# Performance work log

Measured on AMD Instinct MI355X. Metric: run time of the kernel, lower is better.

Reference implementation:

```python
import jax, jax.numpy as jnp
import numpy as np

B, T, C, H = 4, 4096, 1024, 64

def setup_inputs() -> dict:
    key = jax.random.key(0)
    kx, kq, kk, kv = jax.random.split(key, 4)
    x  = jax.random.normal(kx, (B, T, C), dtype=jnp.float32)
    # nn.Linear(C, H, bias=False) weights have shape [H, C]; y = x @ W.T
    Wq = jax.random.normal(kq, (H, C), dtype=jnp.float32) * (C ** -0.5)
    Wk = jax.random.normal(kk, (H, C), dtype=jnp.float32) * (C ** -0.5)
    Wv = jax.random.normal(kv, (H, C), dtype=jnp.float32) * (C ** -0.5)
    return {"x": x, "Wq": Wq, "Wk": Wk, "Wv": Wv}

def reference(x, Wq, Wk, Wv):
    T_ = x.shape[1]
    scale = jnp.asarray(Wq.shape[0] ** -0.5, dtype=x.dtype)
    q = jnp.einsum('btc,hc->bth', x, Wq)
    k = jnp.einsum('btc,hc->bth', x, Wk)
    v = jnp.einsum('btc,hc->bth', x, Wv)
    w = jnp.einsum('bqh,bkh->bqk', q, k)  # [B, T, T] scores
    causal = jnp.tril(jnp.ones((T_, T_), dtype=bool))
    # original: masked_fill(-inf) then scale; -inf * scale == -inf, so equivalent
    w = jnp.where(causal, w * scale, -jnp.inf)
    w = jax.nn.softmax(w, axis=-1)
    # dropout p=0.0 (eval/deterministic): identity
    return jnp.einsum('bqk,bkh->bqh', w, v)
```

## Files before the change

kernel.cpp:

```cpp
#include <hip/hip_runtime.h>
#include <hip/hip_bf16.h>

#define B_ 4
#define T_ 4096
#define C_ 1024

typedef __bf16 bf16_t;
typedef __bf16 bf16x8 __attribute__((ext_vector_type(8)));
typedef float f32x4 __attribute__((ext_vector_type(4)));

__device__ __forceinline__ void gld16(const void* g, void* l) {
    __builtin_amdgcn_global_load_lds((const __attribute__((address_space(1))) void*)g,
                                     (__attribute__((address_space(3))) void*)l, 16, 0, 0);
}

__global__ void wcvt_kernel(const float* __restrict__ Wq, const float* __restrict__ Wk,
                            const float* __restrict__ Wv, bf16_t* __restrict__ wbf) {
    int i = blockIdx.x * 256 + threadIdx.x;
    int m = i >> 16;
    int r = i & 65535;
    const float* src = (m == 0) ? Wq : (m == 1) ? Wk : Wv;
    float s = (m == 0) ? 0.125f * 1.44269504f : 1.0f;
    wbf[i] = (bf16_t)(src[r] * s);
}

__global__ __launch_bounds__(256, 2)
void qkv_proj_kernel(const float* __restrict__ x, const bf16_t* __restrict__ wbf,
                     bf16_t* __restrict__ qb, bf16_t* __restrict__ kb,
                     bf16_t* __restrict__ vtb) {
    __shared__ bf16_t wsb[3][12288];

    const int tid = threadIdx.x;
    const int w = tid >> 6, lane = tid & 63, lr = lane & 15, kg = lane >> 4;
    const int rg = w & 1, cg = w >> 1;
    const int row0 = blockIdx.x * 32;

    const float* xr = x + (size_t)(row0 + rg * 16 + lr) * 1024 + kg * 8;

#define STAGE_W(kk, sl) {                                                           \
        _Pragma("unroll")                                                           \
        for (int j = 0; j < 6; ++j) {                                               \
            int idx = tid + j * 256; int h = idx >> 3, u = idx & 7;                 \
            gld16((const char*)wbf + (size_t)h * 2048 + (size_t)(kk) * 128          \
                      + ((u ^ (h & 7)) * 16),                                       \
                  (char*)&wsb[sl][0] + (size_t)idx * 16); } }
#define LOADX(kk, sl) {                                                             \
        xb[sl][0] = *(const float4*)(xr + (kk) * 64);                               \
        xb[sl][1] = *(const float4*)(xr + (kk) * 64 + 4);                           \
        xb[sl][2] = *(const float4*)(xr + (kk) * 64 + 32);                          \
        xb[sl][3] = *(const float4*)(xr + (kk) * 64 + 36); }

    float4 xb[3][4];
    f32x4 acc[6];
    #pragma unroll
    for (int j = 0; j < 6; ++j) acc[j] = (f32x4){0.f, 0.f, 0.f, 0.f};

    STAGE_W(0, 0); LOADX(0, 0);
    STAGE_W(1, 1); LOADX(1, 1);

    #pragma unroll
    for (int c = 0; c < 16; ++c) {
        if (c < 15) {
            asm volatile("s_waitcnt vmcnt(10)" ::: "memory");
        } else {
            asm volatile("s_waitcnt vmcnt(0)" ::: "memory");
        }
        __builtin_amdgcn_s_barrier();
        if (c + 2 < 16) {
            STAGE_W(c + 2, (c + 2) % 3);
            LOADX(c + 2, (c + 2) % 3);
        }

        {
            const int cur = c % 3;
            const bf16_t* wst = &wsb[cur][0];
            bf16x8 af[2];
            #pragma unroll
            for (int s = 0; s < 2; ++s) {
                float4 a0 = xb[cur][s * 2];
                float4 a1 = xb[cur][s * 2 + 1];
                af[s][0]=(bf16_t)a0.x; af[s][1]=(bf16_t)a0.y;
                af[s][2]=(bf16_t)a0.z; af[s][3]=(bf16_t)a0.w;
                af[s][4]=(bf16_t)a1.x; af[s][5]=(bf16_t)a1.y;
                af[s][6]=(bf16_t)a1.z; af[s][7]=(bf16_t)a1.w;
            }
            __builtin_amdgcn_s_setprio(1);
            #pragma unroll
            for (int j = 0; j < 6; ++j) {
                int p = cg * 6 + j;
                #pragma unroll
                for (int s = 0; s < 2; ++s) {
                    bf16x8 bfr = *(const bf16x8*)&wst[(p * 16 + lr) * 64
                                                      + (((4 * s + kg) ^ (lr & 7)) * 8)];
                    acc[j] = __builtin_amdgcn_mfma_f32_16x16x32_bf16(af[s], bfr, acc[j], 0, 0, 0);
                }
            }
            __builtin_amdgcn_s_setprio(0);
        }
    }

    #pragma unroll
    for (int j = 0; j < 6; ++j) {
        int p = cg * 6 + j;
        int m = p >> 2;
        int h = (p & 3) * 16 + lr;
        #pragma unroll
        for (int i = 0; i < 4; ++i) {
            int t = row0 + rg * 16 + kg * 4 + i;
            float v = acc[j][i];
            if (m == 0) {
                qb[(size_t)t * 64 + h] = (bf16_t)v;
            } else if (m == 1) {
                kb[(size_t)t * 64 + ((((h >> 3) ^ (t & 7)) << 3) | (h & 7))] = (bf16_t)v;
            } else {
                int bb = t >> 12, tt = t & 4095;
                vtb[(size_t)(bb * 64 + h) * 4096 + (tt & ~63)
                    + (((((tt >> 3) & 7) ^ (h & 7))) << 3) + (tt & 7)] = (bf16_t)v;
            }
        }
    }
#undef STAGE_W
#undef LOADX
}

__global__ __launch_bounds__(256, 2)
void attn_kernel(const bf16_t* __restrict__ qb, const bf16_t* __restrict__ kb,
                 const bf16_t* __restrict__ vtb, float* __restrict__ out) {
    __shared__ bf16_t kvb[2][2][8192];
    __shared__ bf16_t p_lds[4][16][68];

    const int tid = threadIdx.x;
    const int w = tid >> 6, lane = tid & 63, lr = lane & 15, kg = lane >> 4;
    const int rg = w & 1, slice = w >> 1;
    const int bid = blockIdx.x;
    const int b = bid & 3;
    const int qt = 127 - (bid >> 2);
    const int qrow0 = qt * 32 + rg * 16;
    const size_t bT = (size_t)b * 4096;

    const int nch    = (qt + 2) >> 1;
    const int nsteps = (nch + 1) >> 1;

#define STAGE_CHUNK(kk, pp, cc) {                                                   \
        _Pragma("unroll")                                                           \
        for (int jj = 0; jj < 2; ++jj) {                                            \
            int idx = tid + jj * 256;                                               \
            gld16((const char*)kb + (bT + (size_t)(kk) * 64) * 128 + (size_t)idx * 16, \
                  (char*)&kvb[pp][cc][0] + (size_t)idx * 16);                       \
            gld16((const char*)vtb + (size_t)(b * 64 + (idx >> 3)) * 8192           \
                      + (size_t)(kk) * 128 + (idx & 7) * 16,                        \
                  (char*)&kvb[pp][cc][4096] + (size_t)idx * 16); } }
#define STAGE_PAIR(j1) {                                                            \
        int c0 = 2 * (j1), c1 = 2 * (j1) + 1, pp = (j1) & 1;                        \
        if (c0 < nch) STAGE_CHUNK(c0, pp, 0);                                       \
        if (c1 < nch) STAGE_CHUNK(c1, pp, 1); }

    bf16x8 qf[2];
    #pragma unroll
    for (int s = 0; s < 2; ++s)
        qf[s] = *(const bf16x8*)&qb[(bT + qrow0 + lr) * 64 + s * 32 + kg * 8];

    f32x4 o_acc[4];
    float l_i[4];
    #pragma unroll
    for (int ct = 0; ct < 4; ++ct) o_acc[ct] = (f32x4){0.f, 0.f, 0.f, 0.f};
    #pragma unroll
    for (int i = 0; i < 4; ++i) l_i[i] = 0.f;

    STAGE_PAIR(0);

    for (int j = 0; j < nsteps; ++j) {
        asm volatile("s_waitcnt vmcnt(0)" ::: "memory");
        __builtin_amdgcn_s_barrier();
        asm volatile("" ::: "memory");
        if (j + 1 < nsteps) STAGE_PAIR(j + 1);

        int c = 2 * j + slice;
        if (c < nch) {
            const bf16_t* Kt = &kvb[j & 1][slice][0];
            const bf16_t* Vt = &kvb[j & 1][slice][4096];
            int kv0 = c * 64;

            f32x4 sc[4];
            #pragma unroll
            for (int ct = 0; ct < 4; ++ct) sc[ct] = (f32x4){0.f, 0.f, 0.f, 0.f};
            __builtin_amdgcn_s_setprio(1);
            #pragma unroll
            for (int ct = 0; ct < 4; ++ct)
                #pragma unroll
                for (int s = 0; s < 2; ++s) {
                    bf16x8 kf = *(const bf16x8*)&Kt[(ct * 16 + lr) * 64 + (((kg + 4 * s) ^ (lr & 7)) * 8)];
                    sc[ct] = __builtin_amdgcn_mfma_f32_16x16x32_bf16(qf[s], kf, sc[ct], 0, 0, 0);
                }
            __builtin_amdgcn_s_setprio(0);

            if (kv0 + 63 > qrow0) {
                #pragma unroll
                for (int ct = 0; ct < 4; ++ct)
                    #pragma unroll
                    for (int i = 0; i < 4; ++i) {
                        int col = kv0 + ct * 16 + lr;
                        int rw  = qrow0 + kg * 4 + i;
                        if (col > rw) sc[ct][i] = -INFINITY;
                    }
            }

            #pragma unroll
            for (int ct = 0; ct < 4; ++ct)
                #pragma unroll
                for (int i = 0; i < 4; ++i) {
                    float p = __builtin_amdgcn_exp2f(sc[ct][i]);
                    p_lds[w][kg * 4 + i][ct * 16 + lr] = (bf16_t)p;
                    l_i[i] += p;
                }

            bf16x8 pf[2];
            #pragma unroll
            for (int s = 0; s < 2; ++s)
                pf[s] = *(const bf16x8*)&p_lds[w][lr][s * 32 + kg * 8];
            __builtin_amdgcn_s_setprio(1);
            #pragma unroll
            for (int ct = 0; ct < 4; ++ct)
                #pragma unroll
                for (int s = 0; s < 2; ++s) {
                    bf16x8 vf = *(const bf16x8*)&Vt[(ct * 16 + lr) * 64 + (((kg + 4 * s) ^ (lr & 7)) * 8)];
                    o_acc[ct] = __builtin_amdgcn_mfma_f32_16x16x32_bf16(pf[s], vf, o_acc[ct], 0, 0, 0);
                }
            __builtin_amdgcn_s_setprio(0);
        }
    }

    asm volatile("s_waitcnt vmcnt(0)" ::: "memory");
    __syncthreads();

    #pragma unroll
    for (int off = 1; off < 16; off <<= 1)
        #pragma unroll
        for (int i = 0; i < 4; ++i)
            l_i[i] += __shfl_xor(l_i[i], off);

    float* co = (float*)&kvb[0][0][0];
    float* cl = co + 2 * 16 * 66;
    if (slice == 1) {
        #pragma unroll
        for (int ct = 0; ct < 4; ++ct)
            #pragma unroll
            for (int i = 0; i < 4; ++i)
                co[(rg * 16 + kg * 4 + i) * 66 + ct * 16 + lr] = o_acc[ct][i];
        if (lr == 0) {
            #pragma unroll
            for (int i = 0; i < 4; ++i)
                cl[rg * 16 + kg * 4 + i] = l_i[i];
        }
    }
    __syncthreads();
    if (slice == 0) {
        #pragma unroll
        for (int i = 0; i < 4; ++i) {
            int r = kg * 4 + i;
            float lv = l_i[i] + cl[rg * 16 + r];
            float inv = 1.0f / lv;
            #pragma unroll
            for (int ct = 0; ct < 4; ++ct) {
                float ov = o_acc[ct][i] + co[(rg * 16 + r) * 66 + ct * 16 + lr];
                out[(bT + qrow0 + r) * 64 + ct * 16 + lr] = ov * inv;
            }
        }
    }
#undef STAGE_CHUNK
#undef STAGE_PAIR
}

extern "C" void kernel_launch(void* const* d_in, const int* in_sizes, int n_in,
                              void* d_out, int out_size, void* d_ws, size_t ws_size,
                              hipStream_t stream) {
    const float* x  = (const float*)d_in[0];
    const float* Wq = (const float*)d_in[1];
    const float* Wk = (const float*)d_in[2];
    const float* Wv = (const float*)d_in[3];
    float* out = (float*)d_out;

    bf16_t* ws  = (bf16_t*)d_ws;
    bf16_t* wbf = ws;
    bf16_t* qb  = ws + 196608;
    bf16_t* kb  = qb + 1048576;
    bf16_t* vtb = kb + 1048576;

    wcvt_kernel<<<768, 256, 0, stream>>>(Wq, Wk, Wv, wbf);
    qkv_proj_kernel<<<512, 256, 0, stream>>>(x, wbf, qb, kb, vtb);
    attn_kernel<<<512, 256, 0, stream>>>(qb, kb, vtb, out);
}
```

Before: 68.69 us.

## Stage x tiles through LDS via async loads with smaller K chunks

The QKV projection now stages x tiles into LDS with async global_load_lds (XOR-swizzled) instead of loading them directly into registers. The K step per iteration is halved (32 instead of 64), so the pipeline runs 32 iterations with smaller per-slot LDS buffers. Occupancy is raised from 2 to 3 blocks per CU. The goal is lower register pressure and more latency hiding, at the cost of more barriers and iterations and extra LDS reads for x.

```diff
diff --git a/kernel.cpp b/kernel.cpp
--- a/kernel.cpp
+++ b/kernel.cpp
@@ -24,76 +24,67 @@
     wbf[i] = (bf16_t)(src[r] * s);
 }
 
-__global__ __launch_bounds__(256, 2)
+__global__ __launch_bounds__(256, 3)
 void qkv_proj_kernel(const float* __restrict__ x, const bf16_t* __restrict__ wbf,
                      bf16_t* __restrict__ qb, bf16_t* __restrict__ kb,
                      bf16_t* __restrict__ vtb) {
-    __shared__ bf16_t wsb[3][12288];
+    __shared__ float  xs[3][1024];
+    __shared__ bf16_t wsb[3][6144];
 
     const int tid = threadIdx.x;
     const int w = tid >> 6, lane = tid & 63, lr = lane & 15, kg = lane >> 4;
     const int rg = w & 1, cg = w >> 1;
     const int row0 = blockIdx.x * 32;
 
-    const float* xr = x + (size_t)(row0 + rg * 16 + lr) * 1024 + kg * 8;
-
+#define STAGE_X(kk, sl) {                                                           \
+        int r = tid >> 3, u = tid & 7;                                              \
+        gld16((const char*)x + (size_t)(row0 + r) * 4096 + (size_t)(kk) * 128       \
+                  + ((u ^ (r & 7)) * 16),                                           \
+              (char*)&xs[sl][0] + (size_t)tid * 16); }
 #define STAGE_W(kk, sl) {                                                           \
         _Pragma("unroll")                                                           \
-        for (int j = 0; j < 6; ++j) {                                               \
-            int idx = tid + j * 256; int h = idx >> 3, u = idx & 7;                 \
-            gld16((const char*)wbf + (size_t)h * 2048 + (size_t)(kk) * 128          \
-                      + ((u ^ (h & 7)) * 16),                                       \
+        for (int j = 0; j < 3; ++j) {                                               \
+            int idx = tid + j * 256; int h = idx >> 2, u = idx & 3;                 \
+            gld16((const char*)wbf + (size_t)h * 2048 + (size_t)(kk) * 64           \
+                      + ((u ^ (h & 3)) * 16),                                       \
                   (char*)&wsb[sl][0] + (size_t)idx * 16); } }
-#define LOADX(kk, sl) {                                                             \
-        xb[sl][0] = *(const float4*)(xr + (kk) * 64);                               \
-        xb[sl][1] = *(const float4*)(xr + (kk) * 64 + 4);                           \
-        xb[sl][2] = *(const float4*)(xr + (kk) * 64 + 32);                          \
-        xb[sl][3] = *(const float4*)(xr + (kk) * 64 + 36); }
-
-    float4 xb[3][4];
+
     f32x4 acc[6];
     #pragma unroll
     for (int j = 0; j < 6; ++j) acc[j] = (f32x4){0.f, 0.f, 0.f, 0.f};
 
-    STAGE_W(0, 0); LOADX(0, 0);
-    STAGE_W(1, 1); LOADX(1, 1);
-
-    #pragma unroll
-    for (int c = 0; c < 16; ++c) {
-        if (c < 15) {
-            asm volatile("s_waitcnt vmcnt(10)" ::: "memory");
+    STAGE_X(0, 0); STAGE_W(0, 0);
+    STAGE_X(1, 1); STAGE_W(1, 1);
+
+    #pragma unroll
+    for (int c = 0; c < 32; ++c) {
+        if (c < 31) {
+            asm volatile("s_waitcnt vmcnt(4)" ::: "memory");
         } else {
             asm volatile("s_waitcnt vmcnt(0)" ::: "memory");
         }
         __builtin_amdgcn_s_barrier();
-        if (c + 2 < 16) {
+        if (c + 2 < 32) {
+            STAGE_X(c + 2, (c + 2) % 3);
             STAGE_W(c + 2, (c + 2) % 3);
-            LOADX(c + 2, (c + 2) % 3);
         }
 
         {
-            const int cur = c % 3;
-            const bf16_t* wst = &wsb[cur][0];
-            bf16x8 af[2];
-            #pragma unroll
-            for (int s = 0; s < 2; ++s) {
-                float4 a0 = xb[cur][s * 2];
-                float4 a1 = xb[cur][s * 2 + 1];
-                af[s][0]=(bf16_t)a0.x; af[s][1]=(bf16_t)a0.y;
-                af[s][2]=(bf16_t)a0.z; af[s][3]=(bf16_t)a0.w;
-                af[s][4]=(bf16_t)a1.x; af[s][5]=(bf16_t)a1.y;
-                af[s][6]=(bf16_t)a1.z; af[s][7]=(bf16_t)a1.w;
-            }
+            const int sl = c % 3;
+            const int rl = rg * 16 + lr;
+            const float* xrow = &xs[sl][rl * 32];
+            float4 f0 = *(const float4*)(xrow + (((kg * 2)     ^ (lr & 7)) * 4));
+            float4 f1 = *(const float4*)(xrow + (((kg * 2 + 1) ^ (lr & 7)) * 4));
+            bf16x8 af;
+            af[0]=(bf16_t)f0.x; af[1]=(bf16_t)f0.y; af[2]=(bf16_t)f0.z; af[3]=(bf16_t)f0.w;
+            af[4]=(bf16_t)f1.x; af[5]=(bf16_t)f1.y; af[6]=(bf16_t)f1.z; af[7]=(bf16_t)f1.w;
+
             __builtin_amdgcn_s_setprio(1);
             #pragma unroll
             for (int j = 0; j < 6; ++j) {
-                int p = cg * 6 + j;
-                #pragma unroll
-                for (int s = 0; s < 2; ++s) {
-                    bf16x8 bfr = *(const bf16x8*)&wst[(p * 16 + lr) * 64
-                                                      + (((4 * s + kg) ^ (lr & 7)) * 8)];
-                    acc[j] = __builtin_amdgcn_mfma_f32_16x16x32_bf16(af[s], bfr, acc[j], 0, 0, 0);
-                }
+                int h = (cg * 6 + j) * 16 + lr;
+                bf16x8 bfr = *(const bf16x8*)&wsb[sl][h * 32 + ((kg ^ (lr & 3)) * 8)];
+                acc[j] = __builtin_amdgcn_mfma_f32_16x16x32_bf16(af, bfr, acc[j], 0, 0, 0);
             }
             __builtin_amdgcn_s_setprio(0);
         }
@@ -119,8 +110,8 @@
             }
         }
     }
+#undef STAGE_X
 #undef STAGE_W
-#undef LOADX
 }
 
 __global__ __launch_bounds__(256, 2)
```

Result: faster. 67.23 us (-2.1%).
